# Optimization experiments

Hardware: AMD Instinct MI355X
Metric: run time of the kernel (lower is better)

The kernel has to match this reference:

```python
import jax, jax.numpy as jnp
import numpy as np

NUM_TRACKS = [128, 256, 512, 1024, 2048, 64, 32, 1024]
B, S, D = 8, 2048, 1536
H = len(NUM_TRACKS)
T = max(NUM_TRACKS)  # num_output_tracks (padded)


def setup_inputs() -> dict:
    key = jax.random.key(0)
    kx, kw, kb, ki = jax.random.split(key, 4)
    x = jax.random.normal(kx, (B, S, D), dtype=jnp.float32)
    # Padded per-species weights: columns >= num_tracks[i] are zero, matching the
    # original's jnp.pad of head logits with zeros.
    track_mask = (jnp.arange(T)[None, :] < jnp.asarray(NUM_TRACKS)[:, None]).astype(jnp.float32)  # [H, T]
    W = jax.random.normal(kw, (H, D, T), dtype=jnp.float32) * 0.02
    W = W * track_mask[:, None, :]
    b = jax.random.normal(kb, (H, T), dtype=jnp.float32) * 0.02
    b = b * track_mask
    head_idx = jax.random.randint(ki, (B,), 0, H, dtype=jnp.int32)
    return {"x": x, "head_idx": head_idx, "W": W, "b": b}


def reference(x, head_idx, W, b):
    # Dense compute of ALL species heads (faithful to original which evaluates
    # every head over the full batch), then per-sample selection via head_idx
    # (equivalent to the original's sequential jnp.where masking).
    logits_all = jnp.einsum('bsd,hdt->bhst', x, W) + b[None, :, None, :]  # [B, H, S, T]
    sel = head_idx[:, None, None, None].astype(jnp.int32)                 # [B, 1, 1, 1]
    logits = jnp.take_along_axis(logits_all, sel, axis=1)[:, 0]           # [B, S, T]
    return logits
```

## Files before the change

### kernel.cpp

```cpp
#include <hip/hip_runtime.h>
#include <hip/hip_bf16.h>
#include <stdint.h>

#define NB 8
#define NS 2048
#define ND 1536
#define NT 2048
#define NH 8

__constant__ int c_nlim[NH] = {128, 256, 512, 1024, 2048, 128, 128, 1024};

typedef short bf16x8 __attribute__((ext_vector_type(8)));
typedef float f32x4 __attribute__((ext_vector_type(4)));

__device__ __forceinline__ unsigned short f2bf(float f) {
    union { float f; unsigned u; } a; a.f = f;
    unsigned r = a.u + 0x7fffu + ((a.u >> 16) & 1u);
    return (unsigned short)(r >> 16);
}

__global__ void cvt_x_kernel(const float* __restrict__ x,
                             unsigned short* __restrict__ xb) {
    const size_t i = (size_t)blockIdx.x * 256 + threadIdx.x;
    float4 v = ((const float4*)x)[i];
    ushort4 o;
    o.x = f2bf(v.x); o.y = f2bf(v.y); o.z = f2bf(v.z); o.w = f2bf(v.w);
    ((ushort4*)xb)[i] = o;
}

__global__ void cvt_w_kernel(const float* __restrict__ W,
                             const int* __restrict__ hidx,
                             unsigned short* __restrict__ Wt) {
    const int h = blockIdx.z;
    bool used = false;
    for (int i = 0; i < NB; ++i) used |= (hidx[i] == h);
    if (!used) return;
    const int t0 = blockIdx.x * 32;
    if (t0 >= c_nlim[h]) return;
    const int d0 = blockIdx.y * 32;

    __shared__ float tile[32][33];
    const int tx = threadIdx.x, ty = threadIdx.y;
#pragma unroll
    for (int i = 0; i < 4; ++i) {
        const int d = d0 + ty + i * 8;
        tile[ty + i * 8][tx] = W[((size_t)h * ND + d) * NT + t0 + tx];
    }
    __syncthreads();
#pragma unroll
    for (int i = 0; i < 4; ++i) {
        const int t = t0 + ty + i * 8;
        Wt[((size_t)h * NT + t) * ND + d0 + tx] = f2bf(tile[tx][ty + i * 8]);
    }
}

#define GLDS(g, l)                                                      \
    __builtin_amdgcn_global_load_lds(                                   \
        (const __attribute__((address_space(1))) void*)(g),             \
        (__attribute__((address_space(3))) void*)(l), 16, 0, 0)

__global__ __launch_bounds__(256) void gemm_kernel(
    const unsigned short* __restrict__ xb,
    const unsigned short* __restrict__ wt,
    const float* __restrict__ bias,
    const int* __restrict__ hidx,
    float* __restrict__ out)
{
    const int batch = blockIdx.z;
    const int m0 = blockIdx.y * 128;
    const int n0 = blockIdx.x * 128;
    const int h = hidx[batch];
    const int tid = threadIdx.x;
    float* outb = out + (size_t)batch * NS * NT;

    if (n0 >= c_nlim[h]) {
        const int row = tid >> 1;
        const int c0 = (tid & 1) * 64;
        float4 z = make_float4(0.f, 0.f, 0.f, 0.f);
        float4* p = (float4*)(outb + (size_t)(m0 + row) * NT + (n0 + c0));
#pragma unroll
        for (int j = 0; j < 16; ++j) p[j] = z;
        return;
    }

    __shared__ unsigned short As[128 * 32];
    __shared__ unsigned short Bs[128 * 32];

    const int lane = tid & 63;
    const int wave = tid >> 6;
    const int wm = (wave >> 1) * 64;
    const int wn = (wave & 1) * 64;
    const int fr = lane & 15;
    const int fq = (lane >> 4) * 8;

    const int r0 = tid >> 2, kc0 = (tid & 3) * 8;
    const int i1 = tid + 256;
    const int r1 = i1 >> 2, kc1 = (i1 & 3) * 8;

    const unsigned short* ga0 = xb + ((size_t)batch * NS + m0 + r0) * ND + kc0;
    const unsigned short* ga1 = xb + ((size_t)batch * NS + m0 + r1) * ND + kc1;
    const unsigned short* gb0 = wt + ((size_t)h * NT + n0 + r0) * ND + kc0;
    const unsigned short* gb1 = wt + ((size_t)h * NT + n0 + r1) * ND + kc1;
    unsigned short* la0 = As + tid * 8;
    unsigned short* la1 = As + i1 * 8;
    unsigned short* lb0 = Bs + tid * 8;
    unsigned short* lb1 = Bs + i1 * 8;

    f32x4 acc[4][4] = {};

    for (int k0 = 0; k0 < ND; k0 += 32) {
        GLDS(ga0, la0); GLDS(ga1, la1); GLDS(gb0, lb0); GLDS(gb1, lb1);
        __syncthreads();
        bf16x8 af[4], bfr[4];
#pragma unroll
        for (int mi = 0; mi < 4; ++mi)
            af[mi] = *(const bf16x8*)(As + (wm + mi * 16 + fr) * 32 + fq);
#pragma unroll
        for (int ni = 0; ni < 4; ++ni)
            bfr[ni] = *(const bf16x8*)(Bs + (wn + ni * 16 + fr) * 32 + fq);
#pragma unroll
        for (int mi = 0; mi < 4; ++mi)
#pragma unroll
            for (int ni = 0; ni < 4; ++ni)
                acc[mi][ni] = __builtin_amdgcn_mfma_f32_16x16x32_bf16(
                    af[mi], bfr[ni], acc[mi][ni], 0, 0, 0);
        __syncthreads();
        ga0 += 32; ga1 += 32; gb0 += 32; gb1 += 32;
    }

    float bv[4];
#pragma unroll
    for (int ni = 0; ni < 4; ++ni)
        bv[ni] = bias[(size_t)h * NT + n0 + wn + ni * 16 + fr];

    const int rbase = m0 + wm + (lane >> 4) * 4;
#pragma unroll
    for (int mi = 0; mi < 4; ++mi) {
#pragma unroll
        for (int r = 0; r < 4; ++r) {
            float* op = outb + (size_t)(rbase + mi * 16 + r) * NT + n0 + wn + fr;
#pragma unroll
            for (int ni = 0; ni < 4; ++ni)
                op[ni * 16] = acc[mi][ni][r] + bv[ni];
        }
    }
}

extern "C" void kernel_launch(void* const* d_in, const int* in_sizes, int n_in,
                              void* d_out, int out_size, void* d_ws, size_t ws_size,
                              hipStream_t stream) {
    const float* x    = (const float*)d_in[0];
    const int*   hidx = (const int*)d_in[1];
    const float* W    = (const float*)d_in[2];
    const float* bias = (const float*)d_in[3];
    float* out = (float*)d_out;

    unsigned short* xb = (unsigned short*)d_ws;
    unsigned short* wt = xb + (size_t)NB * NS * ND;

    cvt_x_kernel<<<dim3(24576), dim3(256), 0, stream>>>(x, xb);
    cvt_w_kernel<<<dim3(NT / 32, ND / 32, NH), dim3(32, 8), 0, stream>>>(W, hidx, wt);
    gemm_kernel<<<dim3(NT / 128, NS / 128, NB), dim3(256), 0, stream>>>(
        xb, wt, bias, hidx, out);
}
```

Before: 374.0 us.

## Double-buffer GEMM LDS tiles and widen W transpose-convert to 64x64 vector stores

The GEMM main loop now uses two LDS buffers and issues the global-to-LDS loads for the next K slice before computing on the current one. This drops one barrier per iteration and lets memory latency overlap with MFMA work. The W transpose/convert kernel moves to 64x64 tiles with float4 loads and 16-byte bf16 stores to cut memory transactions. The cost is doubled shared memory in the GEMM, which may lower occupancy, and the padded 64x69 tile may still leave LDS bank conflicts on the column reads.

After: 405.7 us. 1.08x slower.

```diff
diff --git a/kernel.cpp b/kernel.cpp
--- a/kernel.cpp
+++ b/kernel.cpp
@@ -7,10 +7,12 @@
 #define ND 1536
 #define NT 2048
 #define NH 8
+#define NK (ND / 32)
 
 __constant__ int c_nlim[NH] = {128, 256, 512, 1024, 2048, 128, 128, 1024};
 
 typedef short bf16x8 __attribute__((ext_vector_type(8)));
+typedef unsigned short u16x8 __attribute__((ext_vector_type(8)));
 typedef float f32x4 __attribute__((ext_vector_type(4)));
 
 __device__ __forceinline__ unsigned short f2bf(float f) {
@@ -35,23 +37,30 @@
     bool used = false;
     for (int i = 0; i < NB; ++i) used |= (hidx[i] == h);
     if (!used) return;
-    const int t0 = blockIdx.x * 32;
+    const int t0 = blockIdx.x * 64;
     if (t0 >= c_nlim[h]) return;
-    const int d0 = blockIdx.y * 32;
+    const int d0 = blockIdx.y * 64;
 
-    __shared__ float tile[32][33];
-    const int tx = threadIdx.x, ty = threadIdx.y;
+    __shared__ float tile[64][69];
+    const int tid = threadIdx.x;
 #pragma unroll
     for (int i = 0; i < 4; ++i) {
-        const int d = d0 + ty + i * 8;
-        tile[ty + i * 8][tx] = W[((size_t)h * ND + d) * NT + t0 + tx];
+        const int idx = tid + i * 256;
+        const int d = idx >> 4, c = (idx & 15) * 4;
+        float4 v = *(const float4*)&W[((size_t)h * ND + d0 + d) * NT + t0 + c];
+        tile[d][c] = v.x; tile[d][c + 1] = v.y;
+        tile[d][c + 2] = v.z; tile[d][c + 3] = v.w;
     }
     __syncthreads();
+    const int t = tid >> 2, dc = (tid & 3) * 16;
+    u16x8 o0, o1;
 #pragma unroll
-    for (int i = 0; i < 4; ++i) {
-        const int t = t0 + ty + i * 8;
-        Wt[((size_t)h * NT + t) * ND + d0 + tx] = f2bf(tile[tx][ty + i * 8]);
-    }
+    for (int j = 0; j < 8; ++j) o0[j] = f2bf(tile[dc + j][t]);
+#pragma unroll
+    for (int j = 0; j < 8; ++j) o1[j] = f2bf(tile[dc + 8 + j][t]);
+    unsigned short* p = Wt + ((size_t)h * NT + t0 + t) * ND + d0 + dc;
+    *(u16x8*)p = o0;
+    *(u16x8*)(p + 8) = o1;
 }
 
 #define GLDS(g, l)                                                      \
@@ -83,8 +92,8 @@
         return;
     }
 
-    __shared__ unsigned short As[128 * 32];
-    __shared__ unsigned short Bs[128 * 32];
+    __shared__ unsigned short As[2][128 * 32];
+    __shared__ unsigned short Bs[2][128 * 32];
 
     const int lane = tid & 63;
     const int wave = tid >> 6;
@@ -101,31 +110,34 @@
     const unsigned short* ga1 = xb + ((size_t)batch * NS + m0 + r1) * ND + kc1;
     const unsigned short* gb0 = wt + ((size_t)h * NT + n0 + r0) * ND + kc0;
     const unsigned short* gb1 = wt + ((size_t)h * NT + n0 + r1) * ND + kc1;
-    unsigned short* la0 = As + tid * 8;
-    unsigned short* la1 = As + i1 * 8;
-    unsigned short* lb0 = Bs + tid * 8;
-    unsigned short* lb1 = Bs + i1 * 8;
 
     f32x4 acc[4][4] = {};
 
-    for (int k0 = 0; k0 < ND; k0 += 32) {
-        GLDS(ga0, la0); GLDS(ga1, la1); GLDS(gb0, lb0); GLDS(gb1, lb1);
+    GLDS(ga0, &As[0][tid * 8]); GLDS(ga1, &As[0][i1 * 8]);
+    GLDS(gb0, &Bs[0][tid * 8]); GLDS(gb1, &Bs[0][i1 * 8]);
+
+    for (int it = 0; it < NK; ++it) {
+        const int cur = it & 1;
         __syncthreads();
+        if (it + 1 < NK) {
+            const int nxt = cur ^ 1;
+            ga0 += 32; ga1 += 32; gb0 += 32; gb1 += 32;
+            GLDS(ga0, &As[nxt][tid * 8]); GLDS(ga1, &As[nxt][i1 * 8]);
+            GLDS(gb0, &Bs[nxt][tid * 8]); GLDS(gb1, &Bs[nxt][i1 * 8]);
+        }
         bf16x8 af[4], bfr[4];
 #pragma unroll
         for (int mi = 0; mi < 4; ++mi)
-            af[mi] = *(const bf16x8*)(As + (wm + mi * 16 + fr) * 32 + fq);
+            af[mi] = *(const bf16x8*)(&As[cur][(wm + mi * 16 + fr) * 32 + fq]);
 #pragma unroll
         for (int ni = 0; ni < 4; ++ni)
-            bfr[ni] = *(const bf16x8*)(Bs + (wn + ni * 16 + fr) * 32 + fq);
+            bfr[ni] = *(const bf16x8*)(&Bs[cur][(wn + ni * 16 + fr) * 32 + fq]);
 #pragma unroll
         for (int mi = 0; mi < 4; ++mi)
 #pragma unroll
             for (int ni = 0; ni < 4; ++ni)
                 acc[mi][ni] = __builtin_amdgcn_mfma_f32_16x16x32_bf16(
                     af[mi], bfr[ni], acc[mi][ni], 0, 0, 0);
-        __syncthreads();
-        ga0 += 32; ga1 += 32; gb0 += 32; gb1 += 32;
     }
 
     float bv[4];
@@ -159,7 +171,7 @@
     unsigned short* wt = xb + (size_t)NB * NS * ND;
 
     cvt_x_kernel<<<dim3(24576), dim3(256), 0, stream>>>(x, xb);
-    cvt_w_kernel<<<dim3(NT / 32, ND / 32, NH), dim3(32, 8), 0, stream>>>(W, hidx, wt);
+    cvt_w_kernel<<<dim3(NT / 64, ND / 64, NH), dim3(256), 0, stream>>>(W, hidx, wt);
     gemm_kernel<<<dim3(NT / 128, NS / 128, NB), dim3(256), 0, stream>>>(
         xb, wt, bias, hidx, out);
 }
```
